# Kernel tuning notes

Measured on AMD Instinct MI355X. Metric: run time of the kernel, lower is better.

Reference implementation:

```python
import jax, jax.numpy as jnp
import numpy as np

N = 100_000   # nodes
E = 1_600_000 # edges
D = 128       # feat_dim
H = 128       # hidden dim (both layers)
L = 64        # latent dim
BN_EPS = 1e-5


def setup_inputs() -> dict:
    key = jax.random.key(0)
    ks = jax.random.split(key, 16)
    x = jax.random.normal(ks[0], (N, D), dtype=jnp.float32)
    edge_index = jax.random.randint(ks[1], (2, E), 0, N, dtype=jnp.int64)
    s = 0.05
    return {
        "x": x,
        "edge_index": edge_index,
        # GCN layer 1
        "W1": jax.random.normal(ks[2], (D, H), dtype=jnp.float32) * s,
        "b1": jnp.zeros((H,), dtype=jnp.float32),
        "g1": jnp.ones((H,), dtype=jnp.float32),
        "be1": jnp.zeros((H,), dtype=jnp.float32),
        # GCN layer 2
        "W2": jax.random.normal(ks[3], (H, H), dtype=jnp.float32) * s,
        "b2": jnp.zeros((H,), dtype=jnp.float32),
        "g2": jnp.ones((H,), dtype=jnp.float32),
        "be2": jnp.zeros((H,), dtype=jnp.float32),
        # heads
        "Wmu": jax.random.normal(ks[4], (H, L), dtype=jnp.float32) * s,
        "bmu": jnp.zeros((L,), dtype=jnp.float32),
        "Wlv": jax.random.normal(ks[5], (H, L), dtype=jnp.float32) * s,
        "blv": jnp.zeros((L,), dtype=jnp.float32),
    }


def _gcn_conv(h, src, dst, deg_isqrt, W, b):
    # PyG GCNConv: linear first, then D^{-1/2}(A+I)D^{-1/2} aggregation, then bias.
    hW = h @ W                                   # [N, H]
    norm = deg_isqrt[src] * deg_isqrt[dst]       # [E]
    msg = hW[src] * norm[:, None]                # gather + scale, [E, H]
    agg = jax.ops.segment_sum(msg, dst, num_segments=N)
    # self-loop contribution (norm = deg_isqrt[i]^2)
    agg = agg + hW * (deg_isqrt * deg_isqrt)[:, None]
    return agg + b


def _bn_relu(h, g, be):
    # training-mode BatchNorm1d over the node dim (biased variance), then ReLU
    mean = jnp.mean(h, axis=0)
    var = jnp.mean(jnp.square(h - mean), axis=0)
    hn = (h - mean) * jax.lax.rsqrt(var + BN_EPS) * g + be
    return jax.nn.relu(hn)


def reference(x, edge_index, W1, b1, g1, be1, W2, b2, g2, be2, Wmu, bmu, Wlv, blv):
    src, dst = edge_index[0], edge_index[1]
    # degree with self loops (computed on destination nodes)
    deg = jax.ops.segment_sum(jnp.ones((E,), dtype=x.dtype), dst, num_segments=N) + 1.0
    deg_isqrt = jax.lax.rsqrt(deg)

    h = _bn_relu(_gcn_conv(x, src, dst, deg_isqrt, W1, b1), g1, be1)
    h = _bn_relu(_gcn_conv(h, src, dst, deg_isqrt, W2, b2), g2, be2)
    # dropout is identity in eval mode
    mu = h @ Wmu + bmu
    logvar = h @ Wlv + blv
    return mu, logvar
```

## Files before the change

kernel.cpp:

```cpp
#include <hip/hip_runtime.h>


typedef __attribute__((ext_vector_type(8))) short bf16x8;
typedef __attribute__((ext_vector_type(4))) float f32x4;

#define NB   256
#define PSZ  256
#define PMAX 512

__device__ inline unsigned short f2bf(float f) {
    unsigned u = __float_as_uint(f);
    unsigned r = u + 0x7FFFu + ((u >> 16) & 1u);
    return (unsigned short)(r >> 16);
}
__device__ inline float bf2f(unsigned u16) {
    return __uint_as_float(u16 << 16);
}

__global__ void k_edetect(const int* __restrict__ ei, int n, int* __restrict__ flag) {
    if (threadIdx.x == 0 && blockIdx.x == 0) {
        int is64 = 1;
        for (int i = 0; i < 64; ++i) {
            if (ei[2 * i + 1] != 0 || (unsigned)ei[2 * i] >= (unsigned)n) { is64 = 0; break; }
        }
        *flag = is64;
    }
}

__device__ inline void load_edge(const int* __restrict__ ei, int eflag, size_t i, size_t e,
                                 int& s, int& d) {
    if (eflag) {
        s = ei[2 * i];
        d = ei[2 * e + 2 * i];
    } else {
        s = ei[i];
        d = ei[e + i];
    }
}


__global__ __launch_bounds__(256) void k_hist(const int* __restrict__ ei,
                                              const int* __restrict__ eflag,
                                              unsigned* __restrict__ gh,
                                              int e, int n, int P, int epb) {
    __shared__ unsigned hist[PMAX];
    int t = threadIdx.x, b = blockIdx.x;
    for (int p = t; p < P; p += 256) hist[p] = 0u;
    __syncthreads();
    int f = *eflag;
    int end = min(e, (b + 1) * epb);
    for (int i = b * epb + t; i < end; i += 256) {
        int s, d;
        load_edge(ei, f, (size_t)i, (size_t)e, s, d);
        if ((unsigned)d < (unsigned)n) atomicAdd(&hist[d >> 8], 1u);
    }
    __syncthreads();
    for (int p = t; p < P; p += 256) gh[(size_t)p * NB + b] = hist[p];
}


__global__ __launch_bounds__(256) void k_scanp(const unsigned* __restrict__ gh,
                                               unsigned* __restrict__ boffs,
                                               unsigned* __restrict__ tot, int P) {
    __shared__ unsigned tmp[256];
    int p = blockIdx.x, t = threadIdx.x;
    unsigned v = gh[(size_t)p * NB + t];
    tmp[t] = v;
    __syncthreads();
    for (int o = 1; o < 256; o <<= 1) {
        unsigned u = (t >= o) ? tmp[t - o] : 0u;
        __syncthreads();
        tmp[t] += u;
        __syncthreads();
    }
    boffs[(size_t)p * NB + t] = tmp[t] - v;
    if (t == 255) tot[p] = tmp[255];
}


__global__ void k_scant(const unsigned* __restrict__ tot,
                        unsigned* __restrict__ gofs, int P) {
    __shared__ unsigned tmp[512];
    int t = threadIdx.x;
    unsigned v = (t < P) ? tot[t] : 0u;
    tmp[t] = v;
    __syncthreads();
    for (int o = 1; o < 512; o <<= 1) {
        unsigned u = (t >= o) ? tmp[t - o] : 0u;
        __syncthreads();
        tmp[t] += u;
        __syncthreads();
    }
    if (t < P) gofs[t] = tmp[t] - v;
}


__global__ __launch_bounds__(256) void k_stage(const int* __restrict__ ei,
                                               const int* __restrict__ eflag,
                                               const unsigned* __restrict__ boffs,
                                               const unsigned* __restrict__ gofs,
                                               uint2* __restrict__ staged,
                                               int e, int n, int P, int epb) {
    __shared__ unsigned cur[PMAX];
    int t = threadIdx.x, b = blockIdx.x;
    for (int p = t; p < P; p += 256) cur[p] = gofs[p] + boffs[(size_t)p * NB + b];
    __syncthreads();
    int f = *eflag;
    int end = min(e, (b + 1) * epb);
    for (int i = b * epb + t; i < end; i += 256) {
        int s, d;
        load_edge(ei, f, (size_t)i, (size_t)e, s, d);
        if ((unsigned)d >= (unsigned)n) continue;
        unsigned pos = atomicAdd(&cur[d >> 8], 1u);
        if (pos < (unsigned)e) staged[pos] = make_uint2((unsigned)s, (unsigned)d);
    }
}


__global__ __launch_bounds__(256) void k_fill(const uint2* __restrict__ staged,
                                              const unsigned* __restrict__ gofs,
                                              const unsigned* __restrict__ tot,
                                              int* __restrict__ csr_src,
                                              unsigned* __restrict__ deg,
                                              float* __restrict__ dis,
                                              unsigned* __restrict__ starts,
                                              int n, int P) {
    __shared__ unsigned h2[256], tmp[256], cur2[256];
    int p = blockIdx.x, t = threadIdx.x;
    unsigned base = gofs[p], cnt = tot[p];
    h2[t] = 0u;
    __syncthreads();
    for (unsigned i = t; i < cnt; i += 256) {
        unsigned dl = staged[base + i].y & 255u;
        atomicAdd(&h2[dl], 1u);
    }
    __syncthreads();
    unsigned cv = h2[t];
    tmp[t] = cv;
    __syncthreads();
    for (int o = 1; o < 256; o <<= 1) {
        unsigned u = (t >= o) ? tmp[t - o] : 0u;
        __syncthreads();
        tmp[t] += u;
        __syncthreads();
    }
    unsigned excl = tmp[t] - cv;
    int node = p * PSZ + t;
    if (node < n) {
        deg[node]    = cv;
        dis[node]    = rsqrtf((float)cv + 1.0f);
        starts[node] = base + excl;
    }
    cur2[t] = base + excl;
    __syncthreads();
    for (unsigned i = t; i < cnt; i += 256) {
        uint2 ed = staged[base + i];
        unsigned slot = atomicAdd(&cur2[ed.y & 255u], 1u);
        csr_src[slot] = (ed.x < (unsigned)n) ? (int)ed.x : 0;
    }
}


__global__ __launch_bounds__(256) void prep_weights(const float* __restrict__ W1,
                                                    const float* __restrict__ W2,
                                                    const float* __restrict__ Wmu,
                                                    const float* __restrict__ Wlv,
                                                    const float* __restrict__ bmu,
                                                    const float* __restrict__ blv,
                                                    unsigned short* __restrict__ Wt1,
                                                    unsigned short* __restrict__ Wt2,
                                                    unsigned short* __restrict__ Wtc,
                                                    float* __restrict__ bcat) {
    int idx = blockIdx.x * 256 + threadIdx.x;
    if (idx < 16384) {
        int c = idx >> 7, k = idx & 127;
        Wt1[idx] = f2bf(W1[(size_t)k * 128 + c]);
    } else if (idx < 32768) {
        int t = idx - 16384, c = t >> 7, k = t & 127;
        Wt2[t] = f2bf(W2[(size_t)k * 128 + c]);
    } else if (idx < 49152) {
        int t = idx - 32768, c = t >> 7, k = t & 127;
        float v = (c < 64) ? Wmu[(size_t)k * 64 + c] : Wlv[(size_t)k * 64 + (c - 64)];
        Wtc[t] = f2bf(v);
    }
    if (idx < 128) bcat[idx] = (idx < 64) ? bmu[idx] : blv[idx - 64];
}


__global__ __launch_bounds__(256) void aggregate(const unsigned* __restrict__ hWb,
                                                 const int* __restrict__ csr_src,
                                                 const unsigned* __restrict__ starts,
                                                 const unsigned* __restrict__ deg,
                                                 const float* __restrict__ dis,
                                                 const float* __restrict__ bias,
                                                 float* __restrict__ outh, int n) {
    int node = blockIdx.x * 4 + (threadIdx.x >> 6);
    int lane = threadIdx.x & 63;
    if (node >= n) return;
    unsigned s0 = starts[node], dn = deg[node];
    float ax = 0.f, ay = 0.f;
    unsigned j = 0;
    for (; j + 16 <= dn; j += 16) {
        int si[16]; unsigned vv[16];
#pragma unroll
        for (int q = 0; q < 16; ++q) si[q] = csr_src[s0 + j + q];
#pragma unroll
        for (int q = 0; q < 16; ++q) vv[q] = hWb[(size_t)si[q] * 64 + lane];
#pragma unroll
        for (int q = 0; q < 16; ++q) {
            ax += bf2f(vv[q] & 0xFFFFu);
            ay += bf2f(vv[q] >> 16);
        }
    }
    for (; j + 8 <= dn; j += 8) {
        int si[8]; unsigned vv[8];
#pragma unroll
        for (int q = 0; q < 8; ++q) si[q] = csr_src[s0 + j + q];
#pragma unroll
        for (int q = 0; q < 8; ++q) vv[q] = hWb[(size_t)si[q] * 64 + lane];
#pragma unroll
        for (int q = 0; q < 8; ++q) {
            ax += bf2f(vv[q] & 0xFFFFu);
            ay += bf2f(vv[q] >> 16);
        }
    }
    for (; j + 4 <= dn; j += 4) {
        int si[4]; unsigned vv[4];
#pragma unroll
        for (int q = 0; q < 4; ++q) si[q] = csr_src[s0 + j + q];
#pragma unroll
        for (int q = 0; q < 4; ++q) vv[q] = hWb[(size_t)si[q] * 64 + lane];
#pragma unroll
        for (int q = 0; q < 4; ++q) {
            ax += bf2f(vv[q] & 0xFFFFu);
            ay += bf2f(vv[q] >> 16);
        }
    }
    for (; j < dn; ++j) {
        unsigned v = hWb[(size_t)csr_src[s0 + j] * 64 + lane];
        ax += bf2f(v & 0xFFFFu);
        ay += bf2f(v >> 16);
    }
    unsigned vs = hWb[(size_t)node * 64 + lane];
    ax += bf2f(vs & 0xFFFFu);
    ay += bf2f(vs >> 16);
    float dii = dis[node];
    float rx = fmaf(dii, ax, bias[lane * 2]);
    float ry = fmaf(dii, ay, bias[lane * 2 + 1]);
    *(float2*)(outh + (size_t)node * 128 + lane * 2) = make_float2(rx, ry);
}


__global__ __launch_bounds__(256) void bn_stats(const float* __restrict__ h,
                                                float* __restrict__ sums, int n) {
    int t  = threadIdx.x;
    int q  = t & 31;
    int sl = t >> 5;
    float s0 = 0.f, s1 = 0.f, s2 = 0.f, s3 = 0.f;
    float q0 = 0.f, q1 = 0.f, q2 = 0.f, q3 = 0.f;
    for (int r = blockIdx.x * 8 + sl; r < n; r += gridDim.x * 8) {
        float4 v = *(const float4*)(h + (size_t)r * 128 + q * 4);
        s0 += v.x; q0 = fmaf(v.x, v.x, q0);
        s1 += v.y; q1 = fmaf(v.y, v.y, q1);
        s2 += v.z; q2 = fmaf(v.z, v.z, q2);
        s3 += v.w; q3 = fmaf(v.w, v.w, q3);
    }
    __shared__ float sh[256][8];
    sh[t][0] = s0; sh[t][1] = s1; sh[t][2] = s2; sh[t][3] = s3;
    sh[t][4] = q0; sh[t][5] = q1; sh[t][6] = q2; sh[t][7] = q3;
    __syncthreads();
    if (t < 128) {
        int cq = t >> 2, ce = t & 3;
        float a = 0.f, b = 0.f;
#pragma unroll
        for (int s8 = 0; s8 < 8; ++s8) {
            a += sh[s8 * 32 + cq][ce];
            b += sh[s8 * 32 + cq][4 + ce];
        }
        atomicAdd(&sums[t], a);
        atomicAdd(&sums[128 + t], b);
    }
}

__global__ void bn_final(const float* __restrict__ sums, const float* __restrict__ g,
                         const float* __restrict__ be, float* __restrict__ bnp, int n) {
    int c = threadIdx.x;
    float inv_n = 1.0f / (float)n;
    float mean = sums[c] * inv_n;
    float var  = sums[128 + c] * inv_n - mean * mean;
    float sc   = g[c] * rsqrtf(var + 1e-5f);
    bnp[c]       = sc;
    bnp[128 + c] = be[c] - mean * sc;
}


template <bool HEAD>
__global__ __launch_bounds__(256, 4) void gemm_mfma(const float* __restrict__ A,
                                                    const unsigned short* __restrict__ Wt,
                                                    const float* __restrict__ bnp,
                                                    const float* __restrict__ bias,
                                                    const float* __restrict__ disv,
                                                    void* __restrict__ Cv, int nrows) {
    __shared__ float Cl[64][130];
    __shared__ float bnsc[128], bnsh[128];

    const int tid  = threadIdx.x;
    const int lane = tid & 63;
    const int wv   = tid >> 6;
    const int rowbase = blockIdx.x * 64;
    const bool has_bn = (bnp != nullptr);
    if (has_bn && tid < 128) {
        bnsc[tid] = bnp[tid];
        bnsh[tid] = bnp[128 + tid];
    }
    __syncthreads();

    const int ar = rowbase + wv * 16 + (lane & 15);
    const int kg = (lane >> 4) * 8;
    const int bc = lane & 15;

    f32x4 acc[8];
#pragma unroll
    for (int t = 0; t < 8; ++t) acc[t] = {0.f, 0.f, 0.f, 0.f};

#pragma unroll
    for (int k0 = 0; k0 < 128; k0 += 32) {
        float va[8];
        if (ar < nrows) {
            float4 a0 = *(const float4*)(A + (size_t)ar * 128 + k0 + kg);
            float4 a1 = *(const float4*)(A + (size_t)ar * 128 + k0 + kg + 4);
            va[0] = a0.x; va[1] = a0.y; va[2] = a0.z; va[3] = a0.w;
            va[4] = a1.x; va[5] = a1.y; va[6] = a1.z; va[7] = a1.w;
        } else {
#pragma unroll
            for (int i = 0; i < 8; ++i) va[i] = 0.f;
        }
        if (has_bn) {
#pragma unroll
            for (int i = 0; i < 8; ++i) {
                int k = k0 + kg + i;
                va[i] = fmaxf(0.f, fmaf(va[i], bnsc[k], bnsh[k]));
            }
        }
        bf16x8 af;
#pragma unroll
        for (int i = 0; i < 8; ++i) af[i] = (short)f2bf(va[i]);

#pragma unroll
        for (int ct = 0; ct < 8; ++ct) {
            bf16x8 bf = *(const bf16x8*)(Wt + (size_t)(ct * 16 + bc) * 128 + k0 + kg);
            acc[ct] = __builtin_amdgcn_mfma_f32_16x16x32_bf16(af, bf, acc[ct], 0, 0, 0);
        }
    }

    const int lr = wv * 16 + ((lane >> 4) << 2);
#pragma unroll
    for (int ct = 0; ct < 8; ++ct)
#pragma unroll
        for (int r = 0; r < 4; ++r)
            Cl[lr + r][ct * 16 + bc] = acc[ct][r];
    __syncthreads();

    const int row = tid >> 2;
    const int c0  = (tid & 3) * 32;
    const int gr  = rowbase + row;
    if (gr < nrows) {
        if (!HEAD) {
            float dsc = disv[gr];
            unsigned* C = (unsigned*)Cv;
#pragma unroll
            for (int u = 0; u < 4; ++u) {
                int cb = c0 + u * 8;
                unsigned o0 = (unsigned)f2bf(Cl[row][cb + 0] * dsc) | ((unsigned)f2bf(Cl[row][cb + 1] * dsc) << 16);
                unsigned o1 = (unsigned)f2bf(Cl[row][cb + 2] * dsc) | ((unsigned)f2bf(Cl[row][cb + 3] * dsc) << 16);
                unsigned o2 = (unsigned)f2bf(Cl[row][cb + 4] * dsc) | ((unsigned)f2bf(Cl[row][cb + 5] * dsc) << 16);
                unsigned o3 = (unsigned)f2bf(Cl[row][cb + 6] * dsc) | ((unsigned)f2bf(Cl[row][cb + 7] * dsc) << 16);
                uint4 o4 = {o0, o1, o2, o3};
                *(uint4*)(C + (size_t)gr * 64 + cb / 2) = o4;
            }
        } else {
            float* mu = (float*)Cv;
            float* lv = mu + (size_t)nrows * 64;
            float* dst = (c0 < 64) ? (mu + (size_t)gr * 64 + c0) : (lv + (size_t)gr * 64 + (c0 - 64));
#pragma unroll
            for (int u = 0; u < 8; ++u) {
                int cb = c0 + u * 4;
                float4 o = make_float4(Cl[row][cb + 0] + bias[cb + 0],
                                       Cl[row][cb + 1] + bias[cb + 1],
                                       Cl[row][cb + 2] + bias[cb + 2],
                                       Cl[row][cb + 3] + bias[cb + 3]);
                *(float4*)(dst + u * 4) = o;
            }
        }
    }
}


extern "C" void kernel_launch(void* const* d_in, const int* in_sizes, int n_in,
                              void* d_out, int out_size, void* d_ws, size_t ws_size,
                              hipStream_t stream) {
    const float* x   = (const float*)d_in[0];
    const int*   ei  = (const int*)d_in[1];
    const float* W1  = (const float*)d_in[2];
    const float* b1  = (const float*)d_in[3];
    const float* g1  = (const float*)d_in[4];
    const float* be1 = (const float*)d_in[5];
    const float* W2  = (const float*)d_in[6];
    const float* b2  = (const float*)d_in[7];
    const float* g2  = (const float*)d_in[8];
    const float* be2 = (const float*)d_in[9];
    const float* Wmu = (const float*)d_in[10];
    const float* bmu = (const float*)d_in[11];
    const float* Wlv = (const float*)d_in[12];
    const float* blv = (const float*)d_in[13];

    const int n = in_sizes[0] / 128;
    const int e = in_sizes[1] / 2;

    const int P   = (n + PSZ - 1) / PSZ;
    const int epb = (e + NB - 1) / NB;

    char* ws = (char*)d_ws;
    size_t off = 0;
    auto alloc = [&](size_t bytes) {
        void* p = ws + off;
        off = (off + bytes + 255) & ~(size_t)255;
        return p;
    };
    float*          bufH    = (float*)alloc((size_t)n * 128 * 4);
    unsigned*       hWb     = (unsigned*)alloc((size_t)n * 64 * 4);
    uint2*          staged  = (uint2*)alloc((size_t)e * 8);
    int*            csr_src = (int*)alloc((size_t)e * 4);
    unsigned*       gh      = (unsigned*)alloc((size_t)P * NB * 4);
    unsigned*       boffs   = (unsigned*)alloc((size_t)P * NB * 4);
    unsigned*       tot     = (unsigned*)alloc((size_t)P * 4);
    unsigned*       gofs    = (unsigned*)alloc((size_t)P * 4);
    unsigned*       deg     = (unsigned*)alloc((size_t)n * 4);
    float*          dis     = (float*)alloc((size_t)n * 4);
    unsigned*       starts  = (unsigned*)alloc((size_t)n * 4);
    int*            eflag   = (int*)alloc(256);
    float*          sums    = (float*)alloc(256 * 4);
    float*          bnp     = (float*)alloc(256 * 4);
    unsigned short* Wt1     = (unsigned short*)alloc(16384 * 2);
    unsigned short* Wt2     = (unsigned short*)alloc(16384 * 2);
    unsigned short* Wtc     = (unsigned short*)alloc(16384 * 2);
    float*          bcat    = (float*)alloc(128 * 4);

    const int ab = (n + 3) / 4;
    const int gg = (n + 63) / 64;

    prep_weights<<<192, 256, 0, stream>>>(W1, W2, Wmu, Wlv, bmu, blv, Wt1, Wt2, Wtc, bcat);
    k_edetect<<<1, 64, 0, stream>>>(ei, n, eflag);
    k_hist <<<NB, 256, 0, stream>>>(ei, eflag, gh, e, n, P, epb);
    k_scanp<<<P, 256, 0, stream>>>(gh, boffs, tot, P);
    k_scant<<<1, 512, 0, stream>>>(tot, gofs, P);
    k_stage<<<NB, 256, 0, stream>>>(ei, eflag, boffs, gofs, staged, e, n, P, epb);
    k_fill <<<P, 256, 0, stream>>>(staged, gofs, tot, csr_src, deg, dis, starts, n, P);

    gemm_mfma<false><<<gg, 256, 0, stream>>>(x, Wt1, nullptr, nullptr, dis, hWb, n);
    aggregate<<<ab, 256, 0, stream>>>(hWb, csr_src, starts, deg, dis, b1, bufH, n);
    hipMemsetAsync(sums, 0, 1024, stream);
    bn_stats<<<512, 256, 0, stream>>>(bufH, sums, n);
    bn_final<<<1, 128, 0, stream>>>(sums, g1, be1, bnp, n);

    gemm_mfma<false><<<gg, 256, 0, stream>>>(bufH, Wt2, bnp, nullptr, dis, hWb, n);
    aggregate<<<ab, 256, 0, stream>>>(hWb, csr_src, starts, deg, dis, b2, bufH, n);
    hipMemsetAsync(sums, 0, 1024, stream);
    bn_stats<<<512, 256, 0, stream>>>(bufH, sums, n);
    bn_final<<<1, 128, 0, stream>>>(sums, g2, be2, bnp, n);

    gemm_mfma<true><<<gg, 256, 0, stream>>>(bufH, Wtc, bnp, bcat, nullptr, d_out, n);
}
```

Measured before the change: 389.3 us.

## Slice bf16 hidden features by channel group and pack staged edges into one word

The GEMM epilogue now writes the bf16 hidden features as 8 channel slices of 16 channels each (32 bytes per node per slice). The aggregation kernel assigns each block to one slice of 32 nodes, with 8 lanes per node, so a slice's working set (about 3.2 MB) can stay in cache during random neighbour gathers. Separately, staged edges are packed into one 32-bit word (source index plus the low 8 bits of the destination), which halves the staging traffic and assumes n < 2^24. Edges with an out-of-range source are now dropped rather than clamped to node 0, and the 16-wide unrolled gather loop is removed.

```diff
diff --git a/kernel.cpp b/kernel.cpp
--- a/kernel.cpp
+++ b/kernel.cpp
@@ -52,7 +52,8 @@
     for (int i = b * epb + t; i < end; i += 256) {
         int s, d;
         load_edge(ei, f, (size_t)i, (size_t)e, s, d);
-        if ((unsigned)d < (unsigned)n) atomicAdd(&hist[d >> 8], 1u);
+        if ((unsigned)s < (unsigned)n && (unsigned)d < (unsigned)n)
+            atomicAdd(&hist[d >> 8], 1u);
     }
     __syncthreads();
     for (int p = t; p < P; p += 256) gh[(size_t)p * NB + b] = hist[p];
@@ -99,7 +100,7 @@
                                                const int* __restrict__ eflag,
                                                const unsigned* __restrict__ boffs,
                                                const unsigned* __restrict__ gofs,
-                                               uint2* __restrict__ staged,
+                                               unsigned* __restrict__ staged,
                                                int e, int n, int P, int epb) {
     __shared__ unsigned cur[PMAX];
     int t = threadIdx.x, b = blockIdx.x;
@@ -110,14 +111,14 @@
     for (int i = b * epb + t; i < end; i += 256) {
         int s, d;
         load_edge(ei, f, (size_t)i, (size_t)e, s, d);
-        if ((unsigned)d >= (unsigned)n) continue;
+        if ((unsigned)s >= (unsigned)n || (unsigned)d >= (unsigned)n) continue;
         unsigned pos = atomicAdd(&cur[d >> 8], 1u);
-        if (pos < (unsigned)e) staged[pos] = make_uint2((unsigned)s, (unsigned)d);
-    }
-}
-
-
-__global__ __launch_bounds__(256) void k_fill(const uint2* __restrict__ staged,
+        if (pos < (unsigned)e) staged[pos] = (unsigned)s | ((unsigned)(d & 255) << 24);
+    }
+}
+
+
+__global__ __launch_bounds__(256) void k_fill(const unsigned* __restrict__ staged,
                                               const unsigned* __restrict__ gofs,
                                               const unsigned* __restrict__ tot,
                                               int* __restrict__ csr_src,
@@ -131,8 +132,7 @@
     h2[t] = 0u;
     __syncthreads();
     for (unsigned i = t; i < cnt; i += 256) {
-        unsigned dl = staged[base + i].y & 255u;
-        atomicAdd(&h2[dl], 1u);
+        atomicAdd(&h2[staged[base + i] >> 24], 1u);
     }
     __syncthreads();
     unsigned cv = h2[t];
@@ -154,9 +154,9 @@
     cur2[t] = base + excl;
     __syncthreads();
     for (unsigned i = t; i < cnt; i += 256) {
-        uint2 ed = staged[base + i];
-        unsigned slot = atomicAdd(&cur2[ed.y & 255u], 1u);
-        csr_src[slot] = (ed.x < (unsigned)n) ? (int)ed.x : 0;
+        unsigned v = staged[base + i];
+        unsigned slot = atomicAdd(&cur2[v >> 24], 1u);
+        csr_src[slot] = (int)(v & 0x00FFFFFFu);
     }
 }
 
@@ -187,37 +187,29 @@
 }
 
 
-__global__ __launch_bounds__(256) void aggregate(const unsigned* __restrict__ hWb,
+__global__ __launch_bounds__(256) void aggregate(const unsigned* __restrict__ hWs,
                                                  const int* __restrict__ csr_src,
                                                  const unsigned* __restrict__ starts,
                                                  const unsigned* __restrict__ deg,
                                                  const float* __restrict__ dis,
                                                  const float* __restrict__ bias,
                                                  float* __restrict__ outh, int n) {
-    int node = blockIdx.x * 4 + (threadIdx.x >> 6);
-    int lane = threadIdx.x & 63;
+    const int s    = blockIdx.x & 7;
+    const int nb0  = (blockIdx.x >> 3) * 32;
+    const int t    = threadIdx.x;
+    const int node = nb0 + ((t >> 6) << 3) + ((t & 63) >> 3);
+    const int word = t & 7;
     if (node >= n) return;
+    const unsigned* hp = hWs + (size_t)s * n * 8;
     unsigned s0 = starts[node], dn = deg[node];
     float ax = 0.f, ay = 0.f;
     unsigned j = 0;
-    for (; j + 16 <= dn; j += 16) {
-        int si[16]; unsigned vv[16];
-#pragma unroll
-        for (int q = 0; q < 16; ++q) si[q] = csr_src[s0 + j + q];
-#pragma unroll
-        for (int q = 0; q < 16; ++q) vv[q] = hWb[(size_t)si[q] * 64 + lane];
-#pragma unroll
-        for (int q = 0; q < 16; ++q) {
-            ax += bf2f(vv[q] & 0xFFFFu);
-            ay += bf2f(vv[q] >> 16);
-        }
-    }
     for (; j + 8 <= dn; j += 8) {
         int si[8]; unsigned vv[8];
 #pragma unroll
         for (int q = 0; q < 8; ++q) si[q] = csr_src[s0 + j + q];
 #pragma unroll
-        for (int q = 0; q < 8; ++q) vv[q] = hWb[(size_t)si[q] * 64 + lane];
+        for (int q = 0; q < 8; ++q) vv[q] = hp[(size_t)si[q] * 8 + word];
 #pragma unroll
         for (int q = 0; q < 8; ++q) {
             ax += bf2f(vv[q] & 0xFFFFu);
@@ -229,7 +221,7 @@
 #pragma unroll
         for (int q = 0; q < 4; ++q) si[q] = csr_src[s0 + j + q];
 #pragma unroll
-        for (int q = 0; q < 4; ++q) vv[q] = hWb[(size_t)si[q] * 64 + lane];
+        for (int q = 0; q < 4; ++q) vv[q] = hp[(size_t)si[q] * 8 + word];
 #pragma unroll
         for (int q = 0; q < 4; ++q) {
             ax += bf2f(vv[q] & 0xFFFFu);
@@ -237,17 +229,18 @@
         }
     }
     for (; j < dn; ++j) {
-        unsigned v = hWb[(size_t)csr_src[s0 + j] * 64 + lane];
+        unsigned v = hp[(size_t)csr_src[s0 + j] * 8 + word];
         ax += bf2f(v & 0xFFFFu);
         ay += bf2f(v >> 16);
     }
-    unsigned vs = hWb[(size_t)node * 64 + lane];
+    unsigned vs = hp[(size_t)node * 8 + word];
     ax += bf2f(vs & 0xFFFFu);
     ay += bf2f(vs >> 16);
     float dii = dis[node];
-    float rx = fmaf(dii, ax, bias[lane * 2]);
-    float ry = fmaf(dii, ay, bias[lane * 2 + 1]);
-    *(float2*)(outh + (size_t)node * 128 + lane * 2) = make_float2(rx, ry);
+    int ch = s * 16 + word * 2;
+    float rx = fmaf(dii, ax, bias[ch]);
+    float ry = fmaf(dii, ay, bias[ch + 1]);
+    *(float2*)(outh + (size_t)node * 128 + ch) = make_float2(rx, ry);
 }
 
 
@@ -371,12 +364,15 @@
 #pragma unroll
             for (int u = 0; u < 4; ++u) {
                 int cb = c0 + u * 8;
+                int w  = cb >> 1;
+                int sl = w >> 3;
+                int wr = w & 7;
                 unsigned o0 = (unsigned)f2bf(Cl[row][cb + 0] * dsc) | ((unsigned)f2bf(Cl[row][cb + 1] * dsc) << 16);
                 unsigned o1 = (unsigned)f2bf(Cl[row][cb + 2] * dsc) | ((unsigned)f2bf(Cl[row][cb + 3] * dsc) << 16);
                 unsigned o2 = (unsigned)f2bf(Cl[row][cb + 4] * dsc) | ((unsigned)f2bf(Cl[row][cb + 5] * dsc) << 16);
                 unsigned o3 = (unsigned)f2bf(Cl[row][cb + 6] * dsc) | ((unsigned)f2bf(Cl[row][cb + 7] * dsc) << 16);
                 uint4 o4 = {o0, o1, o2, o3};
-                *(uint4*)(C + (size_t)gr * 64 + cb / 2) = o4;
+                *(uint4*)(C + (size_t)sl * nrows * 8 + (size_t)gr * 8 + wr) = o4;
             }
         } else {
             float* mu = (float*)Cv;
@@ -428,8 +424,8 @@
         return p;
     };
     float*          bufH    = (float*)alloc((size_t)n * 128 * 4);
-    unsigned*       hWb     = (unsigned*)alloc((size_t)n * 64 * 4);
-    uint2*          staged  = (uint2*)alloc((size_t)e * 8);
+    unsigned*       hWs     = (unsigned*)alloc((size_t)n * 64 * 4);
+    unsigned*       staged  = (unsigned*)alloc((size_t)e * 4);
     int*            csr_src = (int*)alloc((size_t)e * 4);
     unsigned*       gh      = (unsigned*)alloc((size_t)P * NB * 4);
     unsigned*       boffs   = (unsigned*)alloc((size_t)P * NB * 4);
@@ -446,7 +442,7 @@
     unsigned short* Wtc     = (unsigned short*)alloc(16384 * 2);
     float*          bcat    = (float*)alloc(128 * 4);
 
-    const int ab = (n + 3) / 4;
+    const int ab = ((n + 31) / 32) * 8;
     const int gg = (n + 63) / 64;
 
     prep_weights<<<192, 256, 0, stream>>>(W1, W2, Wmu, Wlv, bmu, blv, Wt1, Wt2, Wtc, bcat);
@@ -457,14 +453,14 @@
     k_stage<<<NB, 256, 0, stream>>>(ei, eflag, boffs, gofs, staged, e, n, P, epb);
     k_fill <<<P, 256, 0, stream>>>(staged, gofs, tot, csr_src, deg, dis, starts, n, P);
 
-    gemm_mfma<false><<<gg, 256, 0, stream>>>(x, Wt1, nullptr, nullptr, dis, hWb, n);
-    aggregate<<<ab, 256, 0, stream>>>(hWb, csr_src, starts, deg, dis, b1, bufH, n);
+    gemm_mfma<false><<<gg, 256, 0, stream>>>(x, Wt1, nullptr, nullptr, dis, hWs, n);
+    aggregate<<<ab, 256, 0, stream>>>(hWs, csr_src, starts, deg, dis, b1, bufH, n);
     hipMemsetAsync(sums, 0, 1024, stream);
     bn_stats<<<512, 256, 0, stream>>>(bufH, sums, n);
     bn_final<<<1, 128, 0, stream>>>(sums, g1, be1, bnp, n);
 
-    gemm_mfma<false><<<gg, 256, 0, stream>>>(bufH, Wt2, bnp, nullptr, dis, hWb, n);
-    aggregate<<<ab, 256, 0, stream>>>(hWb, csr_src, starts, deg, dis, b2, bufH, n);
+    gemm_mfma<false><<<gg, 256, 0, stream>>>(bufH, Wt2, bnp, nullptr, dis, hWs, n);
+    aggregate<<<ab, 256, 0, stream>>>(hWs, csr_src, starts, deg, dis, b2, bufH, n);
     hipMemsetAsync(sums, 0, 1024, stream);
     bn_stats<<<512, 256, 0, stream>>>(bufH, sums, n);
     bn_final<<<1, 128, 0, stream>>>(sums, g2, be2, bnp, n);
```

Result: slower. 419.0 us (+7.6%).
